# Kernel tuning notes

Hardware: AMD Instinct MI355X
Metric: run time of the kernel (lower is better)

The kernel has to match this reference:

```python
import jax, jax.numpy as jnp
import numpy as np

NUM_HEADS = 8
NUM_KV_HEADS = 1
HEAD_DIM = 256
ROPE_THETA = 10000.0


def setup_inputs() -> dict:
    key = jax.random.key(0)
    ks = jax.random.split(key, 5)
    B, S, H = 4, 2048, 2048
    hidden_states = jax.random.normal(ks[0], (B, S, H), dtype=jnp.float32)
    # Linear weights stored as (in_features, out_features); y = x @ W
    scale = 0.02
    Wq = jax.random.normal(ks[1], (H, NUM_HEADS * HEAD_DIM), dtype=jnp.float32) * scale
    Wk = jax.random.normal(ks[2], (H, NUM_KV_HEADS * HEAD_DIM), dtype=jnp.float32) * scale
    Wv = jax.random.normal(ks[3], (H, NUM_KV_HEADS * HEAD_DIM), dtype=jnp.float32) * scale
    Wo = jax.random.normal(ks[4], (NUM_HEADS * HEAD_DIM, H), dtype=jnp.float32) * scale
    position_ids = jnp.broadcast_to(jnp.arange(S, dtype=jnp.int64), (B, S))
    return {"hidden_states": hidden_states, "Wq": Wq, "Wk": Wk, "Wv": Wv,
            "Wo": Wo, "position_ids": position_ids}


def _rotate_half(x):
    h = x.shape[-1] // 2
    return jnp.concatenate([-x[..., h:], x[..., :h]], axis=-1)


def _rope_cos_sin(position_ids, head_dim, theta):
    # inv_freq: [head_dim/2]
    inv_freq = 1.0 / (theta ** (jnp.arange(0, head_dim, 2, dtype=jnp.float32) / head_dim))
    freqs = position_ids.astype(jnp.float32)[..., None] * inv_freq  # [B,S,hd/2]
    emb = jnp.concatenate([freqs, freqs], axis=-1)                   # [B,S,hd]
    # shape [B,1,S,hd] to broadcast over heads
    return jnp.cos(emb)[:, None], jnp.sin(emb)[:, None]


def reference(hidden_states, Wq, Wk, Wv, Wo, position_ids):
    B, S, H = hidden_states.shape
    groups = NUM_HEADS // NUM_KV_HEADS

    q = (hidden_states @ Wq).reshape(B, S, NUM_HEADS, HEAD_DIM).transpose(0, 2, 1, 3)
    k = (hidden_states @ Wk).reshape(B, S, NUM_KV_HEADS, HEAD_DIM).transpose(0, 2, 1, 3)
    v = (hidden_states @ Wv).reshape(B, S, NUM_KV_HEADS, HEAD_DIM).transpose(0, 2, 1, 3)

    cos, sin = _rope_cos_sin(position_ids, HEAD_DIM, ROPE_THETA)
    q = q * cos + _rotate_half(q) * sin
    k = k * cos + _rotate_half(k) * sin

    # GQA: repeat kv heads to match query heads
    k = jnp.repeat(k, groups, axis=1)  # [B,Hq,S,hd]
    v = jnp.repeat(v, groups, axis=1)

    scores = jnp.einsum('bhqd,bhkd->bhqk', q, k) / jnp.sqrt(jnp.float32(HEAD_DIM))
    causal = position_ids[:, None, :, None] >= position_ids[:, None, None, :]  # [B,1,S,S]
    scores = jnp.where(causal, scores, jnp.float32(-1e9))
    attn = jax.nn.softmax(scores, axis=-1)

    out = jnp.einsum('bhqk,bhkd->bhqd', attn, v)             # [B,H,S,hd]
    out = out.transpose(0, 2, 1, 3).reshape(B, S, NUM_HEADS * HEAD_DIM)
    return out @ Wo
```

## Files before the change

### kernel.cpp

```cpp
#include <hip/hip_runtime.h>
#include <hip/hip_bf16.h>

typedef __bf16 bf16;
typedef __bf16 bf16x8 __attribute__((ext_vector_type(8)));
typedef __bf16 bf16x4 __attribute__((ext_vector_type(4)));
typedef float f32x4 __attribute__((ext_vector_type(4)));

#define NB 4
#define SEQ 2048
#define HID 2048
#define NHEAD 8
#define HDIM 256
#define MTOT (NB*SEQ)

#define WAIT_VM8()  asm volatile("s_waitcnt vmcnt(8)" ::: "memory")
#define WAIT_VM0()  asm volatile("s_waitcnt vmcnt(0)" ::: "memory")

__device__ __forceinline__ void gl_lds16(const void* g, void* l) {
  __builtin_amdgcn_global_load_lds(
      (const __attribute__((address_space(1))) void*)g,
      (__attribute__((address_space(3))) void*)l, 16, 0, 0);
}

__global__ __launch_bounds__(256)
void prologue_kernel(const float* __restrict__ hs, bf16* __restrict__ Xb,
                     const float* __restrict__ Wq, bf16* __restrict__ WqT,
                     const float* __restrict__ Wo, bf16* __restrict__ WoT,
                     const float* __restrict__ Wk, bf16* __restrict__ WkT,
                     const float* __restrict__ Wv, bf16* __restrict__ WvT,
                     float2* __restrict__ tab)
{
  __shared__ float tile[32][33];
  const int bid = blockIdx.x;
  const int t = threadIdx.x;

  if (bid < 8192) {
    size_t i = (size_t)(bid * 256 + t) * 8;
    float4 v0 = *(const float4*)(hs + i);
    float4 v1 = *(const float4*)(hs + i + 4);
    bf16x8 o;
    o[0]=(bf16)v0.x; o[1]=(bf16)v0.y; o[2]=(bf16)v0.z; o[3]=(bf16)v0.w;
    o[4]=(bf16)v1.x; o[5]=(bf16)v1.y; o[6]=(bf16)v1.z; o[7]=(bf16)v1.w;
    *(bf16x8*)(Xb + i) = o;
  } else if (bid < 17408) {
    const float* in; bf16* out; int R, C, bx, by;
    if (bid < 16384) {
      int id = bid - 8192;
      int z = id >> 12, r = id & 4095;
      in = z ? Wo : Wq; out = z ? WoT : WqT; R = 2048; C = 2048;
      bx = (r & 63) * 32; by = (r >> 6) * 32;
    } else {
      int id = bid - 16384;
      int z = id >> 9, r = id & 511;
      in = z ? Wv : Wk; out = z ? WvT : WkT; R = 2048; C = 256;
      bx = (r & 7) * 32; by = (r >> 3) * 32;
    }
    int tx = t & 31, ty = t >> 5;
    #pragma unroll
    for (int k = 0; k < 4; k++)
      tile[ty + 8*k][tx] = in[(size_t)(by + ty + 8*k) * C + bx + tx];
    __syncthreads();
    #pragma unroll
    for (int k = 0; k < 4; k++)
      out[(size_t)(bx + ty + 8*k) * R + by + tx] = (bf16)tile[tx][ty + 8*k];
  } else {
    int i = (bid - 17408) * 256 + t;
    int s = i >> 7, p = i & 127;
    float invf = powf(10000.0f, -(float)p * (1.0f / 128.0f));
    float ang = (float)s * invf;
    float sn, cs;
    sincosf(ang, &sn, &cs);
    tab[i] = make_float2(cs, sn);
  }
}

template<int HEADS>
__global__ void rope_apply_kernel(bf16* __restrict__ X, const float2* __restrict__ tab) {
  int i = blockIdx.x * 256 + threadIdx.x;
  int row = i / (HEADS * 32);
  int rem = i - row * (HEADS * 32);
  int h = rem >> 5;
  int p4 = (rem & 31) * 4;
  int s = row & (SEQ - 1);
  bf16* base = X + (size_t)row * (HEADS * HDIM) + h * HDIM;
  bf16x4 lo = *(bf16x4*)(base + p4);
  bf16x4 hi = *(bf16x4*)(base + p4 + 128);
  bf16x4 nlo, nhi;
  #pragma unroll
  for (int k = 0; k < 4; k++) {
    float2 cs = tab[s * 128 + p4 + k];
    float x0 = (float)lo[k], x1 = (float)hi[k];
    nlo[k] = (bf16)(x0 * cs.x - x1 * cs.y);
    nhi[k] = (bf16)(x1 * cs.x + x0 * cs.y);
  }
  *(bf16x4*)(base + p4) = nlo;
  *(bf16x4*)(base + p4 + 128) = nhi;
}

template<int EPI>
__global__ __launch_bounds__(256, 3)
void gemm_bt_kernel(const bf16* __restrict__ A, const bf16* __restrict__ Bt,
                    void* __restrict__ Cout, int N, int K,
                    bf16* __restrict__ Kout, bf16* __restrict__ VTout)
{
  __shared__ bf16 Abuf[128 * 32];
  __shared__ bf16 Bbuf[128 * 32];
  const int t = threadIdx.x;
  const int lane = t & 63, w = t >> 6;
  const int g = lane >> 4, c = lane & 15;
  const int wm = w >> 1, wn = w & 1;
  const int m0 = blockIdx.y * 128, n0 = blockIdx.x * 128;

  f32x4 acc[4][4];
  #pragma unroll
  for (int i = 0; i < 4; i++)
    #pragma unroll
    for (int j = 0; j < 4; j++)
      acc[i][j] = (f32x4){0.f, 0.f, 0.f, 0.f};

  for (int k0 = 0; k0 < K; k0 += 32) {
    #pragma unroll
    for (int it = 0; it < 2; ++it) {
      int row = it * 64 + (t >> 2);
      int part = (t & 3) ^ (row & 3);
      gl_lds16(A  + (size_t)(m0 + row) * K + k0 + part * 8, Abuf + (it * 256 + w * 64) * 8);
      gl_lds16(Bt + (size_t)(n0 + row) * K + k0 + part * 8, Bbuf + (it * 256 + w * 64) * 8);
    }
    __syncthreads();
    bf16x8 af[4], bfr[4];
    #pragma unroll
    for (int i = 0; i < 4; i++) {
      int row = wm * 64 + i * 16 + c;
      af[i] = *(const bf16x8*)((const char*)Abuf + row * 64 + ((g * 16) ^ ((c & 3) * 16)));
    }
    #pragma unroll
    for (int j = 0; j < 4; j++) {
      int row = wn * 64 + j * 16 + c;
      bfr[j] = *(const bf16x8*)((const char*)Bbuf + row * 64 + ((g * 16) ^ ((c & 3) * 16)));
    }
    #pragma unroll
    for (int i = 0; i < 4; i++)
      #pragma unroll
      for (int j = 0; j < 4; j++)
        acc[i][j] = __builtin_amdgcn_mfma_f32_16x16x32_bf16(af[i], bfr[j], acc[i][j], 0, 0, 0);
    __syncthreads();
  }

  #pragma unroll
  for (int i = 0; i < 4; i++) {
    #pragma unroll
    for (int j = 0; j < 4; j++) {
      #pragma unroll
      for (int rr = 0; rr < 4; rr++) {
        int m = m0 + wm * 64 + i * 16 + g * 4 + rr;
        int col = n0 + wn * 64 + j * 16 + c;
        float v = acc[i][j][rr];
        if constexpr (EPI == 0) {
          ((bf16*)Cout)[(size_t)m * N + col] = (bf16)v;
        } else if constexpr (EPI == 2) {
          ((float*)Cout)[(size_t)m * N + col] = v;
        } else {
          if (col < 256) {
            Kout[(size_t)m * 256 + col] = (bf16)v;
          } else {
            int b = m >> 11, s = m & 2047;
            VTout[((size_t)b * 256 + (col - 256)) * SEQ + s] = (bf16)v;
          }
        }
      }
    }
  }
}

template<int EPI>
__global__ __launch_bounds__(512, 2)
void gemm256_kernel(const bf16* __restrict__ A, const bf16* __restrict__ Bt,
                    void* __restrict__ Cout, int N, int K,
                    const float2* __restrict__ tab)
{
  __shared__ bf16 Albs[2][256 * 64];
  __shared__ bf16 Blbs[2][256 * 64];
  const int t = threadIdx.x, lane = t & 63, w = t >> 6;
  const int g = lane >> 4, c = lane & 15;
  const int wm = w >> 2, wn = w & 3;
  const int m0 = blockIdx.y * 256, n0 = blockIdx.x * 256;

  const bf16* Ab = A + (size_t)m0 * K;
  const bf16* Bb = Bt + (size_t)n0 * K;

  auto stage = [&](const bf16* G, int k0, bf16* lds) {
    #pragma unroll
    for (int it = 0; it < 4; ++it) {
      int slot = it * 512 + t;
      int row = slot >> 3, part = (slot & 7) ^ (row & 7);
      gl_lds16(G + (size_t)row * K + k0 + part * 8, lds + (it * 512 + w * 64) * 8);
    }
  };

  f32x4 acc[8][4];
  #pragma unroll
  for (int i = 0; i < 8; i++)
    #pragma unroll
    for (int j = 0; j < 4; j++)
      acc[i][j] = (f32x4){0.f, 0.f, 0.f, 0.f};

  stage(Ab, 0, &Albs[0][0]);
  stage(Bb, 0, &Blbs[0][0]);
  __builtin_amdgcn_sched_barrier(0);

  const int NT = K >> 6;
  #pragma unroll 1
  for (int kt = 0; kt < NT; ++kt) {
    const int buf = kt & 1;
    if (kt + 1 < NT) {
      stage(Ab, (kt + 1) * 64, &Albs[buf ^ 1][0]);
      stage(Bb, (kt + 1) * 64, &Blbs[buf ^ 1][0]);
    }
    __builtin_amdgcn_sched_barrier(0);
    if (kt + 1 < NT) { WAIT_VM8(); } else { WAIT_VM0(); }
    __builtin_amdgcn_s_barrier();
    __builtin_amdgcn_sched_barrier(0);

    #pragma unroll
    for (int s2 = 0; s2 < 2; s2++) {
      bf16x8 bfr[4];
      #pragma unroll
      for (int j = 0; j < 4; j++) {
        int row = (EPI == 3) ? (wn * 16 + (j & 1) * 64 + (j >> 1) * 128 + c)
                             : (wn * 64 + j * 16 + c);
        bfr[j] = *(const bf16x8*)((const char*)&Blbs[buf][0] + row * 128 +
                                  ((s2 * 64 + g * 16) ^ ((c & 7) * 16)));
      }
      #pragma unroll
      for (int i = 0; i < 8; i++) {
        int row = wm * 128 + i * 16 + c;
        const bf16x8 af = *(const bf16x8*)((const char*)&Albs[buf][0] + row * 128 +
                                           ((s2 * 64 + g * 16) ^ ((c & 7) * 16)));
        #pragma unroll
        for (int j = 0; j < 4; j++)
          acc[i][j] = __builtin_amdgcn_mfma_f32_16x16x32_bf16(af, bfr[j], acc[i][j], 0, 0, 0);
      }
    }
    __builtin_amdgcn_s_barrier();
  }

  if constexpr (EPI == 3) {
    #pragma unroll
    for (int i = 0; i < 8; i++) {
      #pragma unroll
      for (int rr = 0; rr < 4; rr++) {
        int m = m0 + wm * 128 + i * 16 + g * 4 + rr;
        int s = m & (SEQ - 1);
        bf16* orow = (bf16*)Cout + (size_t)m * N + n0;
        #pragma unroll
        for (int jp = 0; jp < 2; jp++) {
          int d = wn * 16 + jp * 64 + c;
          float2 cs = tab[s * 128 + d];
          float vlo = acc[i][jp][rr], vhi = acc[i][jp | 2][rr];
          orow[d]       = (bf16)(vlo * cs.x - vhi * cs.y);
          orow[d + 128] = (bf16)(vhi * cs.x + vlo * cs.y);
        }
      }
    }
  } else {
    #pragma unroll
    for (int i = 0; i < 8; i++) {
      #pragma unroll
      for (int j = 0; j < 4; j++) {
        #pragma unroll
        for (int rr = 0; rr < 4; rr++) {
          int m = m0 + wm * 128 + i * 16 + g * 4 + rr;
          int col = n0 + wn * 64 + j * 16 + c;
          float v = acc[i][j][rr];
          if constexpr (EPI == 0) ((bf16*)Cout)[(size_t)m * N + col] = (bf16)v;
          else                    ((float*)Cout)[(size_t)m * N + col] = v;
        }
      }
    }
  }
}

__global__ __launch_bounds__(512, 2)
void attn_kernel(const bf16* __restrict__ Q, const bf16* __restrict__ Kb,
                 const bf16* __restrict__ VT, bf16* __restrict__ O)
{
  __shared__ bf16 Klds[2][64 * 256];
  __shared__ bf16 Vlds[2][256 * 64];
  __shared__ bf16 Plds[8][16 * 64];

  const int L = blockIdx.x + ((int)gridDim.x) * blockIdx.y;
  const int xcd = L & 7, slot = L >> 3;
  const int b = xcd >> 1;
  const int rem = ((xcd & 1) << 5) | slot;
  const int h = rem >> 3;
  const int p = rem & 7;

  const int t = threadIdx.x, lane = t & 63, w = t >> 6;
  const int g = lane >> 4, c = lane & 15;

  const bf16* Kbase = Kb + (size_t)b * SEQ * HDIM;
  const bf16* Vbase = VT + (size_t)b * HDIM * SEQ;

  bf16x8 ones8;
  #pragma unroll
  for (int z = 0; z < 8; z++) ones8[z] = (bf16)1.0f;

  auto stageK = [&](int kt, int buf) {
    const int kv0 = kt * 64;
    #pragma unroll
    for (int it = 0; it < 4; ++it) {
      int slot2 = it * 512 + t;
      int krow = slot2 >> 5, kpart = (slot2 & 31) ^ (krow & 7);
      gl_lds16(Kbase + (size_t)(kv0 + krow) * HDIM + kpart * 8,
               &Klds[buf][0] + (it * 512 + w * 64) * 8);
    }
  };
  auto stageV = [&](int kt, int buf) {
    const int kv0 = kt * 64;
    #pragma unroll
    for (int it = 0; it < 4; ++it) {
      int slot2 = it * 512 + t;
      int vrow = slot2 >> 3, vpart = (slot2 & 7) ^ (vrow & 7);
      gl_lds16(Vbase + (size_t)vrow * SEQ + kv0 + vpart * 8,
               &Vlds[buf][0] + (it * 512 + w * 64) * 8);
    }
  };

  #pragma unroll 1
  for (int pass = 0; pass < 2; ++pass) {
    const int qt = pass ? (15 - p) : p;
    const int q0 = qt * 128;
    const int last = 2 * qt + 1;

    bf16x8 qf[8];
    const bf16* qp = Q + (size_t)(b * SEQ + q0 + w * 16 + c) * (NHEAD * HDIM) + h * HDIM + g * 8;
    #pragma unroll
    for (int s = 0; s < 8; s++) qf[s] = *(const bf16x8*)(qp + s * 32);
    __builtin_amdgcn_sched_barrier(0);

    stageK(0, 0);
    stageV(0, 0);
    __builtin_amdgcn_sched_barrier(0);

    f32x4 acc[16];
    #pragma unroll
    for (int f = 0; f < 16; f++) acc[f] = (f32x4){0.f, 0.f, 0.f, 0.f};
    f32x4 acc_s = (f32x4){0.f, 0.f, 0.f, 0.f};

    #pragma unroll 1
    for (int kt = 0; kt <= last; ++kt) {
      const int kv0 = kt * 64;
      const int buf = kt & 1;

      if (kt < last) { stageK(kt + 1, buf ^ 1); stageV(kt + 1, buf ^ 1); }
      __builtin_amdgcn_sched_barrier(0);
      if (kt < last) { WAIT_VM8(); } else { WAIT_VM0(); }
      __builtin_amdgcn_s_barrier();
      __builtin_amdgcn_sched_barrier(0);

      const int qrow_min = q0 + w * 16;
      if (kv0 <= qrow_min + 15) {
        f32x4 sc[4];
        #pragma unroll
        for (int j = 0; j < 4; j++) sc[j] = (f32x4){0.f, 0.f, 0.f, 0.f};
        __builtin_amdgcn_s_setprio(1);
        #pragma unroll
        for (int s = 0; s < 8; s++) {
          #pragma unroll
          for (int j = 0; j < 4; j++) {
            const bf16x8 kf = *(const bf16x8*)((const char*)&Klds[buf][0] + (j * 16 + c) * 512 +
                                               ((s * 64 + g * 16) ^ ((c & 7) * 16)));
            sc[j] = __builtin_amdgcn_mfma_f32_16x16x32_bf16(qf[s], kf, sc[j], 0, 0, 0);
          }
        }
        __builtin_amdgcn_s_setprio(0);

        const float C1 = 0.09016844f;
        const float C2 = 11.54156036f;
        const bool diag = (kv0 + 63 > qrow_min);
        #pragma unroll
        for (int rr = 0; rr < 4; rr++) {
          const int row = g * 4 + rr;
          const int qrow = qrow_min + row;
          #pragma unroll
          for (int j = 0; j < 4; j++) {
            float e = exp2f(__builtin_fmaf(sc[j][rr], C1, -C2));
            if (diag && (kv0 + j * 16 + c > qrow)) e = 0.f;
            *(bf16*)((char*)&Plds[w][0] + row * 128 + (((j * 32) + c * 2) ^ ((row & 7) << 4))) = (bf16)e;
          }
        }

        #pragma unroll
        for (int s2 = 0; s2 < 2; s2++) {
          const bf16x8 pf = *(const bf16x8*)((const char*)&Plds[w][0] + c * 128 +
                                             (((s2 * 4 + g) << 4) ^ ((c & 7) << 4)));
          __builtin_amdgcn_s_setprio(1);
          #pragma unroll
          for (int f = 0; f < 16; f++) {
            const bf16x8 vf = *(const bf16x8*)((const char*)&Vlds[buf][0] + (f * 16 + c) * 128 +
                                               ((s2 * 64 + g * 16) ^ ((c & 7) * 16)));
            acc[f] = __builtin_amdgcn_mfma_f32_16x16x32_bf16(pf, vf, acc[f], 0, 0, 0);
          }
          acc_s = __builtin_amdgcn_mfma_f32_16x16x32_bf16(pf, ones8, acc_s, 0, 0, 0);
          __builtin_amdgcn_s_setprio(0);
        }
      }

      __builtin_amdgcn_s_barrier();
    }

    #pragma unroll
    for (int rr = 0; rr < 4; rr++) {
      float inv = 1.0f / acc_s[rr];
      #pragma unroll
      for (int f = 0; f < 16; f++) {
        float v = acc[f][rr] * inv;
        O[(size_t)(b * SEQ + q0 + w * 16 + g * 4 + rr) * (NHEAD * HDIM) + h * HDIM + f * 16 + c] = (bf16)v;
      }
    }
  }
}

extern "C" void kernel_launch(void* const* d_in, const int* in_sizes, int n_in,
                              void* d_out, int out_size, void* d_ws, size_t ws_size,
                              hipStream_t stream) {
  const float* hs = (const float*)d_in[0];
  const float* Wq = (const float*)d_in[1];
  const float* Wk = (const float*)d_in[2];
  const float* Wv = (const float*)d_in[3];
  const float* Wo = (const float*)d_in[4];

  char* ws = (char*)d_ws;
  bf16* Xb   = (bf16*)(ws + 0);
  bf16* WqT  = (bf16*)(ws + 33554432);
  bf16* WkT  = (bf16*)(ws + 41943040);
  bf16* WvT  = (bf16*)(ws + 42991616);
  bf16* WoT  = (bf16*)(ws + 44040192);
  bf16* Qb   = (bf16*)(ws + 52428800);
  bf16* Kb   = (bf16*)(ws + 85983232);
  bf16* VTb  = (bf16*)(ws + 90177536);
  float2* tab = (float2*)(ws + 94371840);

  prologue_kernel<<<18432, 256, 0, stream>>>(hs, Xb, Wq, WqT, Wo, WoT,
                                             Wk, WkT, Wv, WvT, tab);

  gemm256_kernel<3><<<dim3(8, 32), 512, 0, stream>>>(Xb, WqT, (void*)Qb, 2048, 2048, tab);
  gemm_bt_kernel<1><<<dim3(4, 64), 256, 0, stream>>>(Xb, WkT, nullptr, 512, 2048, Kb, VTb);

  rope_apply_kernel<1><<<1024, 256, 0, stream>>>(Kb, tab);

  attn_kernel<<<dim3(8, 32), 512, 0, stream>>>(Qb, Kb, VTb, Xb );

  gemm256_kernel<2><<<dim3(8, 32), 512, 0, stream>>>(Xb, WoT, d_out, 2048, 2048, nullptr);
}
```

Measured before the change: 324.5 us.

## Restructure GEMM main loop into four-phase LDS-read/MFMA schedule with priority hints

Splits each K-tile iteration of the bf16 GEMM into four quadrant phases. Each phase loads only the needed A/B fragments from LDS, then runs a block of MFMAs at raised wave priority with s_setprio, separated by barriers. The next tile's global-to-LDS staging is issued after the first fragment reads rather than before, with a full vmcnt wait before the last quadrant. The goal is to interleave LDS reads, global loads and matrix math across waves, in the style of ping-pong scheduling, at the cost of more barriers per iteration and different register pressure.

```diff
diff --git a/kernel.cpp b/kernel.cpp
--- a/kernel.cpp
+++ b/kernel.cpp
@@ -15,6 +15,7 @@
 
 #define WAIT_VM8()  asm volatile("s_waitcnt vmcnt(8)" ::: "memory")
 #define WAIT_VM0()  asm volatile("s_waitcnt vmcnt(0)" ::: "memory")
+#define LGKM0()     asm volatile("s_waitcnt lgkmcnt(0)" ::: "memory")
 
 __device__ __forceinline__ void gl_lds16(const void* g, void* l) {
   __builtin_amdgcn_global_load_lds(
@@ -196,6 +197,17 @@
       gl_lds16(G + (size_t)row * K + k0 + part * 8, lds + (it * 512 + w * 64) * 8);
     }
   };
+  auto readA = [&](int buf, int i, int s2) -> bf16x8 {
+    int row = wm * 128 + i * 16 + c;
+    return *(const bf16x8*)((const char*)&Albs[buf][0] + row * 128 +
+                            ((s2 * 64 + g * 16) ^ ((c & 7) * 16)));
+  };
+  auto readB = [&](int buf, int j, int s2) -> bf16x8 {
+    int row = (EPI == 3) ? (wn * 16 + (j & 1) * 64 + (j >> 1) * 128 + c)
+                         : (wn * 64 + j * 16 + c);
+    return *(const bf16x8*)((const char*)&Blbs[buf][0] + row * 128 +
+                            ((s2 * 64 + g * 16) ^ ((c & 7) * 16)));
+  };
 
   f32x4 acc[8][4];
   #pragma unroll
@@ -207,41 +219,99 @@
   stage(Ab, 0, &Albs[0][0]);
   stage(Bb, 0, &Blbs[0][0]);
   __builtin_amdgcn_sched_barrier(0);
+  WAIT_VM0();
+  __builtin_amdgcn_s_barrier();
+  __builtin_amdgcn_sched_barrier(0);
 
   const int NT = K >> 6;
   #pragma unroll 1
-  for (int kt = 0; kt < NT; ++kt) {
-    const int buf = kt & 1;
-    if (kt + 1 < NT) {
-      stage(Ab, (kt + 1) * 64, &Albs[buf ^ 1][0]);
-      stage(Bb, (kt + 1) * 64, &Blbs[buf ^ 1][0]);
-    }
-    __builtin_amdgcn_sched_barrier(0);
-    if (kt + 1 < NT) { WAIT_VM8(); } else { WAIT_VM0(); }
-    __builtin_amdgcn_s_barrier();
-    __builtin_amdgcn_sched_barrier(0);
-
-    #pragma unroll
-    for (int s2 = 0; s2 < 2; s2++) {
-      bf16x8 bfr[4];
-      #pragma unroll
-      for (int j = 0; j < 4; j++) {
-        int row = (EPI == 3) ? (wn * 16 + (j & 1) * 64 + (j >> 1) * 128 + c)
-                             : (wn * 64 + j * 16 + c);
-        bfr[j] = *(const bf16x8*)((const char*)&Blbs[buf][0] + row * 128 +
-                                  ((s2 * 64 + g * 16) ^ ((c & 7) * 16)));
-      }
-      #pragma unroll
-      for (int i = 0; i < 8; i++) {
-        int row = wm * 128 + i * 16 + c;
-        const bf16x8 af = *(const bf16x8*)((const char*)&Albs[buf][0] + row * 128 +
-                                           ((s2 * 64 + g * 16) ^ ((c & 7) * 16)));
-        #pragma unroll
-        for (int j = 0; j < 4; j++)
-          acc[i][j] = __builtin_amdgcn_mfma_f32_16x16x32_bf16(af, bfr[j], acc[i][j], 0, 0, 0);
-      }
-    }
-    __builtin_amdgcn_s_barrier();
+  for (int T = 0; T < NT; ++T) {
+    const int buf = T & 1;
+    const bool more = (T + 1 < NT);
+    bf16x8 a0[4][2], a1[4][2], b0[2][2], b1[2][2];
+
+    #pragma unroll
+    for (int ii = 0; ii < 4; ii++)
+      #pragma unroll
+      for (int ks = 0; ks < 2; ks++) a0[ii][ks] = readA(buf, ii, ks);
+    #pragma unroll
+    for (int jj = 0; jj < 2; jj++)
+      #pragma unroll
+      for (int ks = 0; ks < 2; ks++) b0[jj][ks] = readB(buf, jj, ks);
+    if (more) {
+      stage(Ab, (T + 1) * 64, &Albs[buf ^ 1][0]);
+      stage(Bb, (T + 1) * 64, &Blbs[buf ^ 1][0]);
+    }
+    __builtin_amdgcn_sched_barrier(0);
+    __builtin_amdgcn_s_barrier();
+    LGKM0();
+    __builtin_amdgcn_sched_barrier(0);
+    __builtin_amdgcn_s_setprio(1);
+    #pragma unroll
+    for (int ii = 0; ii < 4; ii++)
+      #pragma unroll
+      for (int jj = 0; jj < 2; jj++)
+        #pragma unroll
+        for (int ks = 0; ks < 2; ks++)
+          acc[ii][jj] = __builtin_amdgcn_mfma_f32_16x16x32_bf16(a0[ii][ks], b0[jj][ks], acc[ii][jj], 0, 0, 0);
+    __builtin_amdgcn_s_setprio(0);
+    __builtin_amdgcn_s_barrier();
+    __builtin_amdgcn_sched_barrier(0);
+
+    #pragma unroll
+    for (int jj = 0; jj < 2; jj++)
+      #pragma unroll
+      for (int ks = 0; ks < 2; ks++) b1[jj][ks] = readB(buf, 2 + jj, ks);
+    __builtin_amdgcn_sched_barrier(0);
+    __builtin_amdgcn_s_barrier();
+    LGKM0();
+    __builtin_amdgcn_sched_barrier(0);
+    __builtin_amdgcn_s_setprio(1);
+    #pragma unroll
+    for (int ii = 0; ii < 4; ii++)
+      #pragma unroll
+      for (int jj = 0; jj < 2; jj++)
+        #pragma unroll
+        for (int ks = 0; ks < 2; ks++)
+          acc[ii][2 + jj] = __builtin_amdgcn_mfma_f32_16x16x32_bf16(a0[ii][ks], b1[jj][ks], acc[ii][2 + jj], 0, 0, 0);
+    __builtin_amdgcn_s_setprio(0);
+    __builtin_amdgcn_s_barrier();
+    __builtin_amdgcn_sched_barrier(0);
+
+    #pragma unroll
+    for (int ii = 0; ii < 4; ii++)
+      #pragma unroll
+      for (int ks = 0; ks < 2; ks++) a1[ii][ks] = readA(buf, 4 + ii, ks);
+    __builtin_amdgcn_sched_barrier(0);
+    __builtin_amdgcn_s_barrier();
+    LGKM0();
+    __builtin_amdgcn_sched_barrier(0);
+    __builtin_amdgcn_s_setprio(1);
+    #pragma unroll
+    for (int ii = 0; ii < 4; ii++)
+      #pragma unroll
+      for (int jj = 0; jj < 2; jj++)
+        #pragma unroll
+        for (int ks = 0; ks < 2; ks++)
+          acc[4 + ii][jj] = __builtin_amdgcn_mfma_f32_16x16x32_bf16(a1[ii][ks], b0[jj][ks], acc[4 + ii][jj], 0, 0, 0);
+    __builtin_amdgcn_s_setprio(0);
+    __builtin_amdgcn_s_barrier();
+    __builtin_amdgcn_sched_barrier(0);
+
+    WAIT_VM0();
+    __builtin_amdgcn_s_barrier();
+    __builtin_amdgcn_sched_barrier(0);
+    __builtin_amdgcn_s_setprio(1);
+    #pragma unroll
+    for (int ii = 0; ii < 4; ii++)
+      #pragma unroll
+      for (int jj = 0; jj < 2; jj++)
+        #pragma unroll
+        for (int ks = 0; ks < 2; ks++)
+          acc[4 + ii][2 + jj] = __builtin_amdgcn_mfma_f32_16x16x32_bf16(a1[ii][ks], b1[jj][ks], acc[4 + ii][2 + jj], 0, 0, 0);
+    __builtin_amdgcn_s_setprio(0);
+    __builtin_amdgcn_s_barrier();
+    __builtin_amdgcn_sched_barrier(0);
   }
 
   if constexpr (EPI == 3) {
```

After: 325.3 us. Within noise of the previous version (+0.2%).

## Fuse K/V projection and K rope into the Q projection GEMM launch

Applied to the files above, without the earlier changes.

Extends the 256-tile GEMM with an epilogue variant that treats extra grid columns as the K and V projections. K gets rope applied in the epilogue and V is written transposed. This replaces the separate small K/V GEMM and the standalone rope kernel, removing two launches and a read-modify-write pass over K. The grid grows to 320 blocks, which may leave a partial second wave.

```diff
diff --git a/kernel.cpp b/kernel.cpp
--- a/kernel.cpp
+++ b/kernel.cpp
@@ -74,119 +74,27 @@
   }
 }
 
-template<int HEADS>
-__global__ void rope_apply_kernel(bf16* __restrict__ X, const float2* __restrict__ tab) {
-  int i = blockIdx.x * 256 + threadIdx.x;
-  int row = i / (HEADS * 32);
-  int rem = i - row * (HEADS * 32);
-  int h = rem >> 5;
-  int p4 = (rem & 31) * 4;
-  int s = row & (SEQ - 1);
-  bf16* base = X + (size_t)row * (HEADS * HDIM) + h * HDIM;
-  bf16x4 lo = *(bf16x4*)(base + p4);
-  bf16x4 hi = *(bf16x4*)(base + p4 + 128);
-  bf16x4 nlo, nhi;
-  #pragma unroll
-  for (int k = 0; k < 4; k++) {
-    float2 cs = tab[s * 128 + p4 + k];
-    float x0 = (float)lo[k], x1 = (float)hi[k];
-    nlo[k] = (bf16)(x0 * cs.x - x1 * cs.y);
-    nhi[k] = (bf16)(x1 * cs.x + x0 * cs.y);
-  }
-  *(bf16x4*)(base + p4) = nlo;
-  *(bf16x4*)(base + p4 + 128) = nhi;
-}
-
-template<int EPI>
-__global__ __launch_bounds__(256, 3)
-void gemm_bt_kernel(const bf16* __restrict__ A, const bf16* __restrict__ Bt,
-                    void* __restrict__ Cout, int N, int K,
-                    bf16* __restrict__ Kout, bf16* __restrict__ VTout)
-{
-  __shared__ bf16 Abuf[128 * 32];
-  __shared__ bf16 Bbuf[128 * 32];
-  const int t = threadIdx.x;
-  const int lane = t & 63, w = t >> 6;
-  const int g = lane >> 4, c = lane & 15;
-  const int wm = w >> 1, wn = w & 1;
-  const int m0 = blockIdx.y * 128, n0 = blockIdx.x * 128;
-
-  f32x4 acc[4][4];
-  #pragma unroll
-  for (int i = 0; i < 4; i++)
-    #pragma unroll
-    for (int j = 0; j < 4; j++)
-      acc[i][j] = (f32x4){0.f, 0.f, 0.f, 0.f};
-
-  for (int k0 = 0; k0 < K; k0 += 32) {
-    #pragma unroll
-    for (int it = 0; it < 2; ++it) {
-      int row = it * 64 + (t >> 2);
-      int part = (t & 3) ^ (row & 3);
-      gl_lds16(A  + (size_t)(m0 + row) * K + k0 + part * 8, Abuf + (it * 256 + w * 64) * 8);
-      gl_lds16(Bt + (size_t)(n0 + row) * K + k0 + part * 8, Bbuf + (it * 256 + w * 64) * 8);
-    }
-    __syncthreads();
-    bf16x8 af[4], bfr[4];
-    #pragma unroll
-    for (int i = 0; i < 4; i++) {
-      int row = wm * 64 + i * 16 + c;
-      af[i] = *(const bf16x8*)((const char*)Abuf + row * 64 + ((g * 16) ^ ((c & 3) * 16)));
-    }
-    #pragma unroll
-    for (int j = 0; j < 4; j++) {
-      int row = wn * 64 + j * 16 + c;
-      bfr[j] = *(const bf16x8*)((const char*)Bbuf + row * 64 + ((g * 16) ^ ((c & 3) * 16)));
-    }
-    #pragma unroll
-    for (int i = 0; i < 4; i++)
-      #pragma unroll
-      for (int j = 0; j < 4; j++)
-        acc[i][j] = __builtin_amdgcn_mfma_f32_16x16x32_bf16(af[i], bfr[j], acc[i][j], 0, 0, 0);
-    __syncthreads();
-  }
-
-  #pragma unroll
-  for (int i = 0; i < 4; i++) {
-    #pragma unroll
-    for (int j = 0; j < 4; j++) {
-      #pragma unroll
-      for (int rr = 0; rr < 4; rr++) {
-        int m = m0 + wm * 64 + i * 16 + g * 4 + rr;
-        int col = n0 + wn * 64 + j * 16 + c;
-        float v = acc[i][j][rr];
-        if constexpr (EPI == 0) {
-          ((bf16*)Cout)[(size_t)m * N + col] = (bf16)v;
-        } else if constexpr (EPI == 2) {
-          ((float*)Cout)[(size_t)m * N + col] = v;
-        } else {
-          if (col < 256) {
-            Kout[(size_t)m * 256 + col] = (bf16)v;
-          } else {
-            int b = m >> 11, s = m & 2047;
-            VTout[((size_t)b * 256 + (col - 256)) * SEQ + s] = (bf16)v;
-          }
-        }
-      }
-    }
-  }
-}
-
 template<int EPI>
 __global__ __launch_bounds__(512, 2)
 void gemm256_kernel(const bf16* __restrict__ A, const bf16* __restrict__ Bt,
                     void* __restrict__ Cout, int N, int K,
-                    const float2* __restrict__ tab)
+                    const float2* __restrict__ tab,
+                    const bf16* __restrict__ Bt2,
+                    bf16* __restrict__ Kout, bf16* __restrict__ VTout)
 {
   __shared__ bf16 Albs[2][256 * 64];
   __shared__ bf16 Blbs[2][256 * 64];
   const int t = threadIdx.x, lane = t & 63, w = t >> 6;
   const int g = lane >> 4, c = lane & 15;
   const int wm = w >> 2, wn = w & 3;
-  const int m0 = blockIdx.y * 256, n0 = blockIdx.x * 256;
+  const int bx = blockIdx.x;
+  const int m0 = blockIdx.y * 256;
 
   const bf16* Ab = A + (size_t)m0 * K;
-  const bf16* Bb = Bt + (size_t)n0 * K;
+  const bf16* Bb;
+  int n0;
+  if (EPI == 4 && bx >= 8) { Bb = Bt2 + (size_t)(bx - 8) * 256 * K; n0 = (bx - 8) * 256; }
+  else                     { Bb = Bt  + (size_t)bx * 256 * K;       n0 = bx * 256; }
 
   auto stage = [&](const bf16* G, int k0, bf16* lds) {
     #pragma unroll
@@ -226,8 +134,8 @@
       bf16x8 bfr[4];
       #pragma unroll
       for (int j = 0; j < 4; j++) {
-        int row = (EPI == 3) ? (wn * 16 + (j & 1) * 64 + (j >> 1) * 128 + c)
-                             : (wn * 64 + j * 16 + c);
+        int row = (EPI == 3 || EPI == 4) ? (wn * 16 + (j & 1) * 64 + (j >> 1) * 128 + c)
+                                         : (wn * 64 + j * 16 + c);
         bfr[j] = *(const bf16x8*)((const char*)&Blbs[buf][0] + row * 128 +
                                   ((s2 * 64 + g * 16) ^ ((c & 7) * 16)));
       }
@@ -244,21 +152,55 @@
     __builtin_amdgcn_s_barrier();
   }
 
-  if constexpr (EPI == 3) {
-    #pragma unroll
-    for (int i = 0; i < 8; i++) {
-      #pragma unroll
-      for (int rr = 0; rr < 4; rr++) {
-        int m = m0 + wm * 128 + i * 16 + g * 4 + rr;
-        int s = m & (SEQ - 1);
-        bf16* orow = (bf16*)Cout + (size_t)m * N + n0;
-        #pragma unroll
-        for (int jp = 0; jp < 2; jp++) {
-          int d = wn * 16 + jp * 64 + c;
-          float2 cs = tab[s * 128 + d];
-          float vlo = acc[i][jp][rr], vhi = acc[i][jp | 2][rr];
-          orow[d]       = (bf16)(vlo * cs.x - vhi * cs.y);
-          orow[d + 128] = (bf16)(vhi * cs.x + vlo * cs.y);
+  if constexpr (EPI == 4) {
+    if (bx < 8) {
+      #pragma unroll
+      for (int i = 0; i < 8; i++) {
+        #pragma unroll
+        for (int rr = 0; rr < 4; rr++) {
+          int m = m0 + wm * 128 + i * 16 + g * 4 + rr;
+          int s = m & (SEQ - 1);
+          bf16* orow = (bf16*)Cout + (size_t)m * N + n0;
+          #pragma unroll
+          for (int jp = 0; jp < 2; jp++) {
+            int d = wn * 16 + jp * 64 + c;
+            float2 cs = tab[s * 128 + d];
+            float vlo = acc[i][jp][rr], vhi = acc[i][jp | 2][rr];
+            orow[d]       = (bf16)(vlo * cs.x - vhi * cs.y);
+            orow[d + 128] = (bf16)(vhi * cs.x + vlo * cs.y);
+          }
+        }
+      }
+    } else if (bx == 8) {
+      #pragma unroll
+      for (int i = 0; i < 8; i++) {
+        #pragma unroll
+        for (int rr = 0; rr < 4; rr++) {
+          int m = m0 + wm * 128 + i * 16 + g * 4 + rr;
+          int s = m & (SEQ - 1);
+          bf16* orow = Kout + (size_t)m * 256;
+          #pragma unroll
+          for (int jp = 0; jp < 2; jp++) {
+            int d = wn * 16 + jp * 64 + c;
+            float2 cs = tab[s * 128 + d];
+            float vlo = acc[i][jp][rr], vhi = acc[i][jp | 2][rr];
+            orow[d]       = (bf16)(vlo * cs.x - vhi * cs.y);
+            orow[d + 128] = (bf16)(vhi * cs.x + vlo * cs.y);
+          }
+        }
+      }
+    } else {
+      #pragma unroll
+      for (int i = 0; i < 8; i++) {
+        #pragma unroll
+        for (int rr = 0; rr < 4; rr++) {
+          int m = m0 + wm * 128 + i * 16 + g * 4 + rr;
+          int b = m >> 11, s = m & 2047;
+          #pragma unroll
+          for (int j = 0; j < 4; j++) {
+            int cl = wn * 16 + (j & 1) * 64 + (j >> 1) * 128 + c;
+            VTout[((size_t)b * 256 + cl) * SEQ + s] = (bf16)acc[i][j][rr];
+          }
         }
       }
     }
@@ -444,12 +386,11 @@
   prologue_kernel<<<18432, 256, 0, stream>>>(hs, Xb, Wq, WqT, Wo, WoT,
                                              Wk, WkT, Wv, WvT, tab);
 
-  gemm256_kernel<3><<<dim3(8, 32), 512, 0, stream>>>(Xb, WqT, (void*)Qb, 2048, 2048, tab);
-  gemm_bt_kernel<1><<<dim3(4, 64), 256, 0, stream>>>(Xb, WkT, nullptr, 512, 2048, Kb, VTb);
-
-  rope_apply_kernel<1><<<1024, 256, 0, stream>>>(Kb, tab);
+  gemm256_kernel<4><<<dim3(10, 32), 512, 0, stream>>>(Xb, WqT, (void*)Qb, 2048, 2048,
+                                                      tab, WkT, Kb, VTb);
 
   attn_kernel<<<dim3(8, 32), 512, 0, stream>>>(Qb, Kb, VTb, Xb );
 
-  gemm256_kernel<2><<<dim3(8, 32), 512, 0, stream>>>(Xb, WoT, d_out, 2048, 2048, nullptr);
-}
+  gemm256_kernel<2><<<dim3(8, 32), 512, 0, stream>>>(Xb, WoT, d_out, 2048, 2048,
+                                                     nullptr, nullptr, nullptr, nullptr);
+}
```

Result: slower. 354.9 us (+9.3%).
